# Optimization experiments

Hardware: AMD Instinct MI355X
Metric: run time of the kernel (lower is better)

The kernel has to match this reference:

```python
import jax, jax.numpy as jnp
import numpy as np
from jax import lax

NUM_HEADS = 8
EPS = 1e-12  # torch F.normalize default eps


def setup_inputs() -> dict:
    key = jax.random.key(0)
    ks = jax.random.split(key, 7)
    B, C, H, W = 4, 128, 256, 256
    d = C // 2  # per-branch channels = 64
    x = jax.random.normal(ks[0], (B, C, H, W), jnp.float32)
    w_qkv1 = jax.random.normal(ks[1], (3 * d, d), jnp.float32) * 0.05
    w_qkv2 = jax.random.normal(ks[2], (3 * d, d), jnp.float32) * 0.05
    w_dw1 = jax.random.normal(ks[3], (3 * d, 1, 3, 3), jnp.float32) * 0.05
    w_dw2 = jax.random.normal(ks[4], (3 * d, 1, 3, 3), jnp.float32) * 0.05
    w_po1 = jax.random.normal(ks[5], (d, d), jnp.float32) * 0.05
    w_po2 = jax.random.normal(ks[6], (d, d), jnp.float32) * 0.05
    t1 = jnp.ones((NUM_HEADS, 1, 1), jnp.float32)
    t2 = jnp.ones((NUM_HEADS, 1, 1), jnp.float32)
    return {"x": x, "w_qkv1": w_qkv1, "w_qkv2": w_qkv2, "w_dw1": w_dw1,
            "w_dw2": w_dw2, "w_po1": w_po1, "w_po2": w_po2, "t1": t1, "t2": t2}


def _qkv(xb, w1x1, wdw):
    # 1x1 conv (pointwise) then 3x3 depthwise conv, no bias
    y = jnp.einsum('bchw,oc->bohw', xb, w1x1)
    y = lax.conv_general_dilated(
        y, wdw, window_strides=(1, 1), padding='SAME',
        dimension_numbers=('NCHW', 'OIHW', 'NCHW'),
        feature_group_count=y.shape[1])
    return y


def _heads(t, b, h, w):
    # b (head c) h w -> b head c (h*w)
    return t.reshape(b, NUM_HEADS, -1, h * w)


def _l2norm(t):
    n = jnp.sqrt(jnp.sum(t * t, axis=-1, keepdims=True))
    return t / jnp.maximum(n, EPS)


def reference(x, w_qkv1, w_qkv2, w_dw1, w_dw2, w_po1, w_po2, t1, t2):
    b, c, h, w = x.shape
    x1, x2 = jnp.split(x, 2, axis=1)
    q1, k1, v1 = jnp.split(_qkv(x1, w_qkv1, w_dw1), 3, axis=1)
    q2, k2, v2 = jnp.split(_qkv(x2, w_qkv2, w_dw2), 3, axis=1)
    q1, k1, v1 = (_heads(t, b, h, w) for t in (q1, k1, v1))
    q2, k2, v2 = (_heads(t, b, h, w) for t in (q2, k2, v2))
    q1, k1 = _l2norm(q1), _l2norm(k1)
    q2, k2 = _l2norm(q2), _l2norm(k2)
    # channel-wise attention: [b, head, c_h, c_h]
    attn1 = jax.nn.softmax(jnp.einsum('bhcn,bhdn->bhcd', q1, k1) * t1[None], axis=-1)
    attn2 = jax.nn.softmax(jnp.einsum('bhcn,bhdn->bhcd', q2, k2) * t2[None], axis=-1)
    # cross-branch V swap
    out1 = jnp.einsum('bhcd,bhdn->bhcn', attn1, v2).reshape(b, c // 2, h, w)
    out2 = jnp.einsum('bhcd,bhdn->bhcn', attn2, v1).reshape(b, c // 2, h, w)
    out1 = jnp.einsum('bchw,oc->bohw', out1, w_po1)
    out2 = jnp.einsum('bchw,oc->bohw', out2, w_po2)
    return jnp.concatenate([out1, out2], axis=1)
```

## Files before the change

kernel.cpp:

```cpp
#include <hip/hip_runtime.h>
#include <hip/hip_fp16.h>

#define NPIX 65536
#define WIMG 256
#define HIMG 256
#define TW 16
#define TH 8
#define HSTR 24
#define NSLOT 240
#define YCH 248

typedef __attribute__((ext_vector_type(8))) _Float16 half8;
typedef __attribute__((ext_vector_type(4))) float f32x4;

__device__ __forceinline__ unsigned int h2u(__half2 h) {
  union { __half2 h; unsigned int u; } c; c.h = h; return c.u;
}
__device__ __forceinline__ __half2 u2h(unsigned int u) {
  union { unsigned int u; __half2 h; } c; c.u = u; return c.h;
}
__device__ __forceinline__ __half2 sp2(_Float16 s) {
  union { _Float16 h[2]; __half2 v; } u; u.h[0] = s; u.h[1] = s; return u.v;
}
__device__ __forceinline__ int qk_idx(int ch, int pxblk) {
  return ch * 128 + ((pxblk ^ (ch & 7)) << 3);
}
__device__ __forceinline__ void ld16_lds(const void* g, void* l) {
  __builtin_amdgcn_global_load_lds(
      (const __attribute__((address_space(1))) unsigned int*)g,
      (__attribute__((address_space(3))) unsigned int*)l, 16, 0, 0);
}

__global__ __launch_bounds__(256)
void k_prep(const float* __restrict__ wq1, const float* __restrict__ wq2,
            const float* __restrict__ wd1, const float* __restrict__ wd2,
            float* __restrict__ zbuf,
            _Float16* __restrict__ wqh, _Float16* __restrict__ wdh) {
  int i = blockIdx.x * 256 + threadIdx.x;
  if (i < 6144) {
    zbuf[i] = 0.0f;
  } else {
    int j = i - 6144;
    if (j < 24576) {
      int br = j / 12288, r = j - br * 12288;
      wqh[j] = (_Float16)((br ? wq2 : wq1)[r]);
    } else {
      int k = j - 24576;
      int br = k / 3072, r = k - br * 3072;
      int o = r >> 4, t = r & 15;
      wdh[k] = (t < 9) ? (_Float16)((br ? wd2 : wd1)[o * 9 + t]) : (_Float16)0.0f;
    }
  }
}

__global__ __launch_bounds__(256)
void k_xt(const float* __restrict__ x, __half* __restrict__ xT) {
  __shared__ _Float16 tile[64 * 257];
  const int strip = blockIdx.x;
  const int br = blockIdx.y, b = blockIdx.z;
  const int tid = threadIdx.x;
  const float* xb = x + ((size_t)b * 128 + br * 64) * NPIX + strip * 256;
  #pragma unroll 8
  for (int c = 0; c < 64; ++c)
    tile[c * 257 + tid] = (_Float16)xb[(size_t)c * NPIX + tid];
  __syncthreads();
  __half* xo = xT + ((size_t)(b * 2 + br) * NPIX + strip * 256) * 64;
  const int j = tid & 7;
  #pragma unroll
  for (int i = 0; i < 8; ++i) {
    int p = (tid >> 3) + i * 32;
    half8 h;
    #pragma unroll
    for (int k = 0; k < 8; ++k) h[k] = tile[(j * 8 + k) * 257 + p];
    *(half8*)((_Float16*)xo + p * 64 + j * 8) = h;
  }
}

__global__ __launch_bounds__(256, 3)
void k_qkv(const __half* __restrict__ xT,
           const _Float16* __restrict__ wqh, const _Float16* __restrict__ wdh,
           const float* __restrict__ zpage,
           __half* __restrict__ vbuf, float* __restrict__ gram,
           float* __restrict__ sqq, float* __restrict__ sqk)
{
  __shared__ __align__(16) _Float16 xs[256 * 64];
  __shared__ __align__(16) _Float16 ys[32 * YCH];

  const int tid = threadIdx.x;
  const int lane = tid & 63;
  const int wid = tid >> 6;
  const int tile = blockIdx.x;
  const int br = blockIdx.y;
  const int b = blockIdx.z;
  const int tx0 = (tile & 15) * TW;
  const int ty0 = (tile >> 4) * TH;

  const _Float16* wqb = wqh + br * 12288;
  const _Float16* wdb = wdh + br * 3072;
  const __half* xTimg = xT + (size_t)(b * 2 + br) * NPIX * 64;

  {
    const int j = lane & 7, pl = lane >> 3;
    for (int it = wid; it < 30; it += 4) {
      int s = it * 8;
      int slot = s + pl;
      int hy = slot / HSTR;
      int hx = slot - hy * HSTR;
      int gy = ty0 - 1 + hy, gx = tx0 - 1 + hx;
      bool valid = (hx < 18) && ((unsigned)gy < HIMG) && ((unsigned)gx < WIMG);
      const void* src = valid
        ? (const void*)((const _Float16*)xTimg + (size_t)(gy * WIMG + gx) * 64
                        + ((j ^ (slot & 7)) << 3))
        : (const void*)((const char*)zpage + lane * 16);
      ld16_lds(src, (void*)(xs + s * 64));
    }
  }
  asm volatile("s_waitcnt vmcnt(0)" ::: "memory");
  __syncthreads();

  const int col = lane & 15;
  const int qrow = lane >> 4;
  const int oo = tid >> 3;
  const int row = tid & 7;

  unsigned int qreg[2][8], kreg[2][8];

#define LOADW(P_, H_, F00, F01, F10, F11, WV, W8) do {                        \
    const _Float16* wp_ = wqb + ((((P_) * 64 + (H_) * 32 + col) << 6) + qrow * 8); \
    F00 = *(const half8*)(wp_);                                               \
    F10 = *(const half8*)(wp_ + 32);                                          \
    F01 = *(const half8*)(wp_ + 1024);                                        \
    F11 = *(const half8*)(wp_ + 1024 + 32);                                   \
    const _Float16* wdp_ = wdb + ((((P_) * 64 + (H_) * 32 + oo)) << 4);       \
    WV = *(const half8*)wdp_;                                                 \
    W8 = wdp_[8];                                                             \
} while (0)

#define PHASE(P_, H_, F00, F01, F10, F11, WV, W8) do {                        \
    for (int mt = wid; mt < 15; mt += 4) {                                    \
      int px = mt * 16 + col;                                                 \
      half8 af0 = *(const half8*)(xs + px * 64 + (((qrow    ) ^ (px & 7)) << 3)); \
      half8 af1 = *(const half8*)(xs + px * 64 + (((4 + qrow) ^ (px & 7)) << 3)); \
      f32x4 a0 = {0,0,0,0}, a1 = {0,0,0,0};                                   \
      a0 = __builtin_amdgcn_mfma_f32_16x16x32_f16(af0, F00, a0, 0, 0, 0);     \
      a0 = __builtin_amdgcn_mfma_f32_16x16x32_f16(af1, F10, a0, 0, 0, 0);     \
      a1 = __builtin_amdgcn_mfma_f32_16x16x32_f16(af0, F01, a1, 0, 0, 0);     \
      a1 = __builtin_amdgcn_mfma_f32_16x16x32_f16(af1, F11, a1, 0, 0, 0);     \
      int pxd = mt * 16 + qrow * 4;                                           \
      __half2* d0 = (__half2*)(ys + (col     ) * YCH + pxd);                  \
      __half2* d1 = (__half2*)(ys + (col + 16) * YCH + pxd);                  \
      d0[0] = __floats2half2_rn(a0[0], a0[1]);                                \
      d0[1] = __floats2half2_rn(a0[2], a0[3]);                                \
      d1[0] = __floats2half2_rn(a1[0], a1[1]);                                \
      d1[1] = __floats2half2_rn(a1[2], a1[3]);                                \
    }                                                                         \
    __syncthreads();                                                          \
    {                                                                         \
      const int o_ = (H_) * 32 + oo;                                          \
      __half2 w2_[9];                                                         \
      _Pragma("unroll")                                                       \
      for (int j = 0; j < 8; ++j) w2_[j] = sp2(WV[j]);                        \
      w2_[8] = sp2(W8);                                                       \
      __half2 a_[8];                                                          \
      _Pragma("unroll")                                                       \
      for (int k2 = 0; k2 < 8; ++k2) a_[k2] = u2h(0u);                        \
      _Pragma("unroll")                                                       \
      for (int ky = 0; ky < 3; ++ky) {                                        \
        const _Float16* rp_ = ys + oo * YCH + (row + ky) * HSTR;              \
        uint4 ra_ = *(const uint4*)rp_;                                       \
        uint4 rb_ = *(const uint4*)(rp_ + 8);                                 \
        unsigned int rc_ = *(const unsigned int*)(rp_ + 16);                  \
        unsigned int A_[9] = {ra_.x, ra_.y, ra_.z, ra_.w,                     \
                              rb_.x, rb_.y, rb_.z, rb_.w, rc_};               \
        _Pragma("unroll")                                                     \
        for (int k2 = 0; k2 < 8; ++k2) {                                      \
          unsigned int M_ = (A_[k2] >> 16) | (A_[k2 + 1] << 16);              \
          a_[k2] = __hfma2(w2_[ky * 3 + 0], u2h(A_[k2]), a_[k2]);             \
          a_[k2] = __hfma2(w2_[ky * 3 + 1], u2h(M_), a_[k2]);                 \
          a_[k2] = __hfma2(w2_[ky * 3 + 2], u2h(A_[k2 + 1]), a_[k2]);         \
        }                                                                     \
      }                                                                       \
      if ((P_) == 0) {                                                        \
        _Pragma("unroll")                                                     \
        for (int k2 = 0; k2 < 8; ++k2) qreg[H_][k2] = h2u(a_[k2]);            \
      } else if ((P_) == 1) {                                                 \
        _Pragma("unroll")                                                     \
        for (int k2 = 0; k2 < 8; ++k2) kreg[H_][k2] = h2u(a_[k2]);            \
      } else {                                                                \
        __half* vrow_ = (__half*)(vbuf                                        \
            + ((size_t)((br * 4 + b) * 64 + o_)) * NPIX                       \
            + (ty0 + row) * WIMG + tx0);                                      \
        uint4 s0_ = {h2u(a_[0]), h2u(a_[1]), h2u(a_[2]), h2u(a_[3])};         \
        uint4 s1_ = {h2u(a_[4]), h2u(a_[5]), h2u(a_[6]), h2u(a_[7])};         \
        *(uint4*)vrow_ = s0_;                                                 \
        *(uint4*)(vrow_ + 8) = s1_;                                           \
        if ((H_) == 1) {                                                      \
          _Float16* qsb_ = xs;                                                \
          _Float16* ksb_ = xs + 64 * 128;                                     \
          _Pragma("unroll")                                                   \
          for (int hh = 0; hh < 2; ++hh) {                                    \
            int ch = hh * 32 + oo;                                            \
            uint4 q0_ = {qreg[hh][0], qreg[hh][1], qreg[hh][2], qreg[hh][3]}; \
            uint4 q1_ = {qreg[hh][4], qreg[hh][5], qreg[hh][6], qreg[hh][7]}; \
            uint4 k0_ = {kreg[hh][0], kreg[hh][1], kreg[hh][2], kreg[hh][3]}; \
            uint4 k1_ = {kreg[hh][4], kreg[hh][5], kreg[hh][6], kreg[hh][7]}; \
            *(uint4*)(qsb_ + qk_idx(ch, 2 * row))     = q0_;                  \
            *(uint4*)(qsb_ + qk_idx(ch, 2 * row + 1)) = q1_;                  \
            *(uint4*)(ksb_ + qk_idx(ch, 2 * row))     = k0_;                  \
            *(uint4*)(ksb_ + qk_idx(ch, 2 * row + 1)) = k1_;                  \
          }                                                                   \
        }                                                                     \
      }                                                                       \
    }                                                                         \
    __syncthreads();                                                          \
} while (0)

  half8 Af00, Af01, Af10, Af11, Awv;
  half8 Bf00, Bf01, Bf10, Bf11, Bwv;
  _Float16 Aw8, Bw8;

  LOADW(0, 0, Af00, Af01, Af10, Af11, Awv, Aw8);
  LOADW(0, 1, Bf00, Bf01, Bf10, Bf11, Bwv, Bw8);
  PHASE(0, 0, Af00, Af01, Af10, Af11, Awv, Aw8);
  LOADW(1, 0, Af00, Af01, Af10, Af11, Awv, Aw8);
  PHASE(0, 1, Bf00, Bf01, Bf10, Bf11, Bwv, Bw8);
  LOADW(1, 1, Bf00, Bf01, Bf10, Bf11, Bwv, Bw8);
  PHASE(1, 0, Af00, Af01, Af10, Af11, Awv, Aw8);
  LOADW(2, 0, Af00, Af01, Af10, Af11, Awv, Aw8);
  PHASE(1, 1, Bf00, Bf01, Bf10, Bf11, Bwv, Bw8);
  LOADW(2, 1, Bf00, Bf01, Bf10, Bf11, Bwv, Bw8);
  PHASE(2, 0, Af00, Af01, Af10, Af11, Awv, Aw8);
  PHASE(2, 1, Bf00, Bf01, Bf10, Bf11, Bwv, Bw8);

  {
    const _Float16* qsb = xs;
    const _Float16* ksb = xs + 64 * 128;
    f32x4 gqk = {0,0,0,0}, gqq = {0,0,0,0}, gkk = {0,0,0,0};
    int ch = wid * 16 + col;
    #pragma unroll
    for (int kc = 0; kc < 4; ++kc) {
      int pb = kc * 4 + qrow;
      half8 aq = *(const half8*)(qsb + qk_idx(ch, pb));
      half8 bk = *(const half8*)(ksb + qk_idx(ch, pb));
      gqk = __builtin_amdgcn_mfma_f32_16x16x32_f16(aq, bk, gqk, 0, 0, 0);
      gqq = __builtin_amdgcn_mfma_f32_16x16x32_f16(aq, aq, gqq, 0, 0, 0);
      gkk = __builtin_amdgcn_mfma_f32_16x16x32_f16(bk, bk, gkk, 0, 0, 0);
    }
    const int gb_off = (br * 4 + b);
    if (((lane >> 3) & 1) == (lane >> 5)) {
      float* gb = gram + gb_off * 512;
      int kch = ch;
      int qc0 = wid * 16 + qrow * 4;
      #pragma unroll
      for (int r = 0; r < 4; ++r) {
        int qch = qc0 + r;
        atomicAdd(&gb[(qch >> 3) * 64 + (qch & 7) * 8 + (kch & 7)], gqk[r]);
      }
    }
    if ((col >> 2) == qrow) {
      atomicAdd(&sqq[gb_off * 64 + ch], gqq[lane & 3]);
      atomicAdd(&sqk[gb_off * 64 + ch], gkk[lane & 3]);
    }
  }
#undef LOADW
#undef PHASE
}

__global__ __launch_bounds__(64)
void k_attn(const float* __restrict__ gram, const float* __restrict__ sqq,
            const float* __restrict__ sqk,
            const float* __restrict__ wpo1, const float* __restrict__ wpo2,
            const float* __restrict__ t1, const float* __restrict__ t2,
            _Float16* __restrict__ wefft)
{
  const int br = blockIdx.x, b = blockIdx.y;
  const int t = threadIdx.x;
  __shared__ float attn[8][8][8];
  const float* gb = gram + (br * 4 + b) * 512;
  const float* sq = sqq + (br * 4 + b) * 64;
  const float* sk = sqk + (br * 4 + b) * 64;
  const float* tt = br ? t2 : t1;
  {
    int h = t >> 3, cq = t & 7;
    float ts = tt[h];
    float qn = fmaxf(sqrtf(sq[h * 8 + cq]), 1e-12f);
    float lg[8], m = -1e30f;
    #pragma unroll
    for (int d2 = 0; d2 < 8; ++d2) {
      float kn = fmaxf(sqrtf(sk[h * 8 + d2]), 1e-12f);
      lg[d2] = ts * gb[h * 64 + cq * 8 + d2] / (qn * kn);
      m = fmaxf(m, lg[d2]);
    }
    float s = 0.f;
    #pragma unroll
    for (int d2 = 0; d2 < 8; ++d2) { lg[d2] = expf(lg[d2] - m); s += lg[d2]; }
    float inv = 1.0f / s;
    #pragma unroll
    for (int d2 = 0; d2 < 8; ++d2) attn[h][cq][d2] = lg[d2] * inv;
  }
  __syncthreads();
  const float* wpo = br ? wpo2 : wpo1;
  _Float16* wt = wefft + (br * 4 + b) * 4096;
  for (int cp = 0; cp < 64; ++cp) {
    int hp = cp >> 3, ip = cp & 7;
    float acc = 0.f;
    #pragma unroll
    for (int j = 0; j < 8; ++j)
      acc += wpo[t * 64 + hp * 8 + j] * attn[hp][j][ip];
    wt[t * 64 + cp] = (_Float16)acc;
  }
}

__global__ __launch_bounds__(256)
void k_out(const __half* __restrict__ vbuf, const _Float16* __restrict__ wefft,
           float* __restrict__ out)
{
  __shared__ __align__(16) _Float16 vs[64 * 128];
  __shared__ __align__(16) _Float16 vt[128 * 64];

  const int strip = blockIdx.x;
  const int obr = blockIdx.y, b = blockIdx.z;
  const int brv = 1 - obr;
  const int tid = threadIdx.x;
  const int lane = tid & 63;
  const int wid = tid >> 6;
  const int col = lane & 15;
  const int qrow = lane >> 4;

  const __half* vb = vbuf + ((size_t)(brv * 4 + b) * 64) * NPIX + strip * 128;

  for (int i = 0; i < 4; ++i) {
    int it = wid * 4 + i;
    const void* src = (const void*)((const _Float16*)vb
        + (size_t)(it * 4 + (lane >> 4)) * NPIX + (lane & 15) * 8);
    ld16_lds(src, (void*)(vs + it * 512));
  }
  asm volatile("s_waitcnt vmcnt(0)" ::: "memory");
  __syncthreads();

  {
    int px = tid & 127, cb = tid >> 7;
    #pragma unroll
    for (int j = 0; j < 4; ++j) {
      half8 h;
      #pragma unroll
      for (int e = 0; e < 8; ++e) h[e] = vs[(cb * 32 + j * 8 + e) * 128 + px];
      int chunk = cb * 4 + j;
      *(half8*)(vt + ((px * 8 + (chunk ^ (px & 7))) << 3)) = h;
    }
  }
  __syncthreads();

  const _Float16* wt = wefft + (obr * 4 + b) * 4096;
  half8 bf[2][4];
  #pragma unroll
  for (int nt = 0; nt < 4; ++nt)
    #pragma unroll
    for (int kc = 0; kc < 2; ++kc)
      bf[kc][nt] = *(const half8*)(wt + (nt * 16 + col) * 64 + kc * 32 + qrow * 8);

  float* ob = out + ((size_t)b * 128 + obr * 64) * NPIX + strip * 128;
  #pragma unroll
  for (int mi = 0; mi < 2; ++mi) {
    int mt = wid * 2 + mi;
    int px = mt * 16 + col;
    half8 af0 = *(const half8*)(vt + ((px * 8 + ((qrow    ) ^ (px & 7))) << 3));
    half8 af1 = *(const half8*)(vt + ((px * 8 + ((4 + qrow) ^ (px & 7))) << 3));
    f32x4 acc[4] = {{0,0,0,0},{0,0,0,0},{0,0,0,0},{0,0,0,0}};
    #pragma unroll
    for (int nt = 0; nt < 4; ++nt) {
      acc[nt] = __builtin_amdgcn_mfma_f32_16x16x32_f16(af0, bf[0][nt], acc[nt], 0, 0, 0);
      acc[nt] = __builtin_amdgcn_mfma_f32_16x16x32_f16(af1, bf[1][nt], acc[nt], 0, 0, 0);
    }
    int pxd = mt * 16 + qrow * 4;
    #pragma unroll
    for (int nt = 0; nt < 4; ++nt) {
      float4 s = {acc[nt][0], acc[nt][1], acc[nt][2], acc[nt][3]};
      *(float4*)(ob + (size_t)(nt * 16 + col) * NPIX + pxd) = s;
    }
  }
}

extern "C" void kernel_launch(void* const* d_in, const int* in_sizes, int n_in,
                              void* d_out, int out_size, void* d_ws, size_t ws_size,
                              hipStream_t stream) {
  const float* x     = (const float*)d_in[0];
  const float* wqkv1 = (const float*)d_in[1];
  const float* wqkv2 = (const float*)d_in[2];
  const float* wdw1  = (const float*)d_in[3];
  const float* wdw2  = (const float*)d_in[4];
  const float* wpo1  = (const float*)d_in[5];
  const float* wpo2  = (const float*)d_in[6];
  const float* t1    = (const float*)d_in[7];
  const float* t2    = (const float*)d_in[8];

  char* ws = (char*)d_ws;
  __half* vbuf = (__half*)ws;
  float* gram  = (float*)(ws + 67108864);
  float* sqq   = gram + 4096;
  float* sqk   = sqq + 512;
  float* zpage = sqk + 512;
  _Float16* wqkvh = (_Float16*)(zpage + 1024);
  _Float16* wdwh  = wqkvh + 24576;
  _Float16* wefft = wdwh + 6144;

  __half* xT = (__half*)d_out;

  k_prep<<<dim3(144), dim3(256), 0, stream>>>(wqkv1, wqkv2, wdw1, wdw2,
                                              gram, wqkvh, wdwh);
  k_xt<<<dim3(256, 2, 4), dim3(256), 0, stream>>>(x, xT);
  k_qkv<<<dim3(512, 2, 4), dim3(256), 0, stream>>>(xT, wqkvh, wdwh,
                                                   zpage, vbuf, gram, sqq, sqk);
  k_attn<<<dim3(2, 4), dim3(64), 0, stream>>>(gram, sqq, sqk, wpo1, wpo2, t1, t2, wefft);
  k_out<<<dim3(512, 2, 4), dim3(256), 0, stream>>>(vbuf, wefft, (float*)d_out);
}
```

Measured before the change: 220.8 us.

## Double k_qkv block size to 512 threads, splitting depthwise rows across pairs

k_qkv now runs with 512 threads per block. Each thread computes half of a 16-pixel row in the depthwise 3x3 conv, and the MFMA tile loops and halo loads stride by 8 waves. The gram reduction is split across two wave groups over the pixel-block dimension, which doubles the atomic adds into the gram and norm buffers. The aim is more waves in flight to hide LDS and memory latency and fewer registers per thread, at the cost of twice as many global atomics and lower per-thread ILP.

```diff
diff --git a/kernel.cpp b/kernel.cpp
--- a/kernel.cpp
+++ b/kernel.cpp
@@ -76,7 +76,7 @@
   }
 }
 
-__global__ __launch_bounds__(256, 3)
+__global__ __launch_bounds__(512, 4)
 void k_qkv(const __half* __restrict__ xT,
            const _Float16* __restrict__ wqh, const _Float16* __restrict__ wdh,
            const float* __restrict__ zpage,
@@ -101,7 +101,7 @@
 
   {
     const int j = lane & 7, pl = lane >> 3;
-    for (int it = wid; it < 30; it += 4) {
+    for (int it = wid; it < 30; it += 8) {
       int s = it * 8;
       int slot = s + pl;
       int hy = slot / HSTR;
@@ -120,10 +120,11 @@
 
   const int col = lane & 15;
   const int qrow = lane >> 4;
-  const int oo = tid >> 3;
-  const int row = tid & 7;
-
-  unsigned int qreg[2][8], kreg[2][8];
+  const int oo = tid >> 4;
+  const int row = (tid >> 1) & 7;
+  const int half = tid & 1;
+
+  unsigned int qreg[2][4], kreg[2][4];
 
 #define LOADW(P_, H_, F00, F01, F10, F11, WV, W8) do {                        \
     const _Float16* wp_ = wqb + ((((P_) * 64 + (H_) * 32 + col) << 6) + qrow * 8); \
@@ -137,7 +138,7 @@
 } while (0)
 
 #define PHASE(P_, H_, F00, F01, F10, F11, WV, W8) do {                        \
-    for (int mt = wid; mt < 15; mt += 4) {                                    \
+    for (int mt = wid; mt < 15; mt += 8) {                                    \
       int px = mt * 16 + col;                                                 \
       half8 af0 = *(const half8*)(xs + px * 64 + (((qrow    ) ^ (px & 7)) << 3)); \
       half8 af1 = *(const half8*)(xs + px * 64 + (((4 + qrow) ^ (px & 7)) << 3)); \
@@ -161,53 +162,47 @@
       _Pragma("unroll")                                                       \
       for (int j = 0; j < 8; ++j) w2_[j] = sp2(WV[j]);                        \
       w2_[8] = sp2(W8);                                                       \
-      __half2 a_[8];                                                          \
+      __half2 a_[4];                                                          \
       _Pragma("unroll")                                                       \
-      for (int k2 = 0; k2 < 8; ++k2) a_[k2] = u2h(0u);                        \
+      for (int k2 = 0; k2 < 4; ++k2) a_[k2] = u2h(0u);                        \
       _Pragma("unroll")                                                       \
       for (int ky = 0; ky < 3; ++ky) {                                        \
-        const _Float16* rp_ = ys + oo * YCH + (row + ky) * HSTR;              \
-        uint4 ra_ = *(const uint4*)rp_;                                       \
-        uint4 rb_ = *(const uint4*)(rp_ + 8);                                 \
-        unsigned int rc_ = *(const unsigned int*)(rp_ + 16);                  \
-        unsigned int A_[9] = {ra_.x, ra_.y, ra_.z, ra_.w,                     \
-                              rb_.x, rb_.y, rb_.z, rb_.w, rc_};               \
+        const _Float16* rp_ = ys + oo * YCH + (row + ky) * HSTR + half * 8;   \
+        uint2 ra_ = *(const uint2*)rp_;                                       \
+        uint2 rb_ = *(const uint2*)(rp_ + 4);                                 \
+        unsigned int rc_ = *(const unsigned int*)(rp_ + 8);                   \
+        unsigned int W_[5] = {ra_.x, ra_.y, rb_.x, rb_.y, rc_};               \
         _Pragma("unroll")                                                     \
-        for (int k2 = 0; k2 < 8; ++k2) {                                      \
-          unsigned int M_ = (A_[k2] >> 16) | (A_[k2 + 1] << 16);              \
-          a_[k2] = __hfma2(w2_[ky * 3 + 0], u2h(A_[k2]), a_[k2]);             \
+        for (int k2 = 0; k2 < 4; ++k2) {                                      \
+          unsigned int M_ = (W_[k2] >> 16) | (W_[k2 + 1] << 16);              \
+          a_[k2] = __hfma2(w2_[ky * 3 + 0], u2h(W_[k2]), a_[k2]);             \
           a_[k2] = __hfma2(w2_[ky * 3 + 1], u2h(M_), a_[k2]);                 \
-          a_[k2] = __hfma2(w2_[ky * 3 + 2], u2h(A_[k2 + 1]), a_[k2]);         \
+          a_[k2] = __hfma2(w2_[ky * 3 + 2], u2h(W_[k2 + 1]), a_[k2]);         \
         }                                                                     \
       }                                                                       \
       if ((P_) == 0) {                                                        \
         _Pragma("unroll")                                                     \
-        for (int k2 = 0; k2 < 8; ++k2) qreg[H_][k2] = h2u(a_[k2]);            \
+        for (int k2 = 0; k2 < 4; ++k2) qreg[H_][k2] = h2u(a_[k2]);            \
       } else if ((P_) == 1) {                                                 \
         _Pragma("unroll")                                                     \
-        for (int k2 = 0; k2 < 8; ++k2) kreg[H_][k2] = h2u(a_[k2]);            \
+        for (int k2 = 0; k2 < 4; ++k2) kreg[H_][k2] = h2u(a_[k2]);            \
       } else {                                                                \
         __half* vrow_ = (__half*)(vbuf                                        \
             + ((size_t)((br * 4 + b) * 64 + o_)) * NPIX                       \
-            + (ty0 + row) * WIMG + tx0);                                      \
-        uint4 s0_ = {h2u(a_[0]), h2u(a_[1]), h2u(a_[2]), h2u(a_[3])};         \
-        uint4 s1_ = {h2u(a_[4]), h2u(a_[5]), h2u(a_[6]), h2u(a_[7])};         \
-        *(uint4*)vrow_ = s0_;                                                 \
-        *(uint4*)(vrow_ + 8) = s1_;                                           \
+            + (ty0 + row) * WIMG + tx0 + half * 8);                           \
+        uint4 s_ = {h2u(a_[0]), h2u(a_[1]), h2u(a_[2]), h2u(a_[3])};          \
+        *(uint4*)vrow_ = s_;                                                  \
         if ((H_) == 1) {                                                      \
           _Float16* qsb_ = xs;                                                \
           _Float16* ksb_ = xs + 64 * 128;                                     \
+          const int pb_ = row * 2 + half;                                     \
           _Pragma("unroll")                                                   \
           for (int hh = 0; hh < 2; ++hh) {                                    \
             int ch = hh * 32 + oo;                                            \
-            uint4 q0_ = {qreg[hh][0], qreg[hh][1], qreg[hh][2], qreg[hh][3]}; \
-            uint4 q1_ = {qreg[hh][4], qreg[hh][5], qreg[hh][6], qreg[hh][7]}; \
-            uint4 k0_ = {kreg[hh][0], kreg[hh][1], kreg[hh][2], kreg[hh][3]}; \
-            uint4 k1_ = {kreg[hh][4], kreg[hh][5], kreg[hh][6], kreg[hh][7]}; \
-            *(uint4*)(qsb_ + qk_idx(ch, 2 * row))     = q0_;                  \
-            *(uint4*)(qsb_ + qk_idx(ch, 2 * row + 1)) = q1_;                  \
-            *(uint4*)(ksb_ + qk_idx(ch, 2 * row))     = k0_;                  \
-            *(uint4*)(ksb_ + qk_idx(ch, 2 * row + 1)) = k1_;                  \
+            uint4 q_ = {qreg[hh][0], qreg[hh][1], qreg[hh][2], qreg[hh][3]};  \
+            uint4 k_ = {kreg[hh][0], kreg[hh][1], kreg[hh][2], kreg[hh][3]};  \
+            *(uint4*)(qsb_ + qk_idx(ch, pb_)) = q_;                           \
+            *(uint4*)(ksb_ + qk_idx(ch, pb_)) = k_;                           \
           }                                                                   \
         }                                                                     \
       }                                                                       \
@@ -236,10 +231,11 @@
     const _Float16* qsb = xs;
     const _Float16* ksb = xs + 64 * 128;
     f32x4 gqk = {0,0,0,0}, gqq = {0,0,0,0}, gkk = {0,0,0,0};
-    int ch = wid * 16 + col;
-    #pragma unroll
-    for (int kc = 0; kc < 4; ++kc) {
-      int pb = kc * 4 + qrow;
+    int ch = (wid & 3) * 16 + col;
+    int kcb = (wid >> 2) * 2;
+    #pragma unroll
+    for (int i = 0; i < 2; ++i) {
+      int pb = (kcb + i) * 4 + qrow;
       half8 aq = *(const half8*)(qsb + qk_idx(ch, pb));
       half8 bk = *(const half8*)(ksb + qk_idx(ch, pb));
       gqk = __builtin_amdgcn_mfma_f32_16x16x32_f16(aq, bk, gqk, 0, 0, 0);
@@ -250,7 +246,7 @@
     if (((lane >> 3) & 1) == (lane >> 5)) {
       float* gb = gram + gb_off * 512;
       int kch = ch;
-      int qc0 = wid * 16 + qrow * 4;
+      int qc0 = (wid & 3) * 16 + qrow * 4;
       #pragma unroll
       for (int r = 0; r < 4; ++r) {
         int qch = qc0 + r;
@@ -409,7 +405,7 @@
   k_prep<<<dim3(144), dim3(256), 0, stream>>>(wqkv1, wqkv2, wdw1, wdw2,
                                               gram, wqkvh, wdwh);
   k_xt<<<dim3(256, 2, 4), dim3(256), 0, stream>>>(x, xT);
-  k_qkv<<<dim3(512, 2, 4), dim3(256), 0, stream>>>(xT, wqkvh, wdwh,
+  k_qkv<<<dim3(512, 2, 4), dim3(512), 0, stream>>>(xT, wqkvh, wdwh,
                                                    zpage, vbuf, gram, sqq, sqk);
   k_attn<<<dim3(2, 4), dim3(64), 0, stream>>>(gram, sqq, sqk, wpo1, wpo2, t1, t2, wefft);
   k_out<<<dim3(512, 2, 4), dim3(256), 0, stream>>>(vbuf, wefft, (float*)d_out);
```

New measurement: 335.7 us. 1.52x slower.
